# Kernel optimization log

Hardware: AMD Instinct MI355X
Metric: run time of the kernel (lower is better)

The kernel has to match this reference:

```python
import jax, jax.numpy as jnp
import numpy as np

D = 1024
H = 16
HD = D // H
FF = 4 * D
EPS = 1e-6


def layernorm(x, g, b):
    mu = jnp.mean(x, axis=-1, keepdims=True)
    var = jnp.mean((x - mu) ** 2, axis=-1, keepdims=True)
    return (x - mu) * jax.lax.rsqrt(var + EPS) * g + b


def setup_inputs() -> dict:
    key = jax.random.key(0)
    ks = jax.random.split(key, 12)
    s = 0.02
    return {
        "x": jax.random.normal(ks[0], (8, 1024, D), dtype=jnp.float32),
        "qkv_w": jax.random.normal(ks[1], (3 * D, D), dtype=jnp.float32) * s,
        "qkv_b": jnp.zeros((3 * D,), dtype=jnp.float32),
        "proj_w": jax.random.normal(ks[2], (D, D), dtype=jnp.float32) * s,
        "proj_b": jnp.zeros((D,), dtype=jnp.float32),
        "fc1_w": jax.random.normal(ks[3], (FF, D), dtype=jnp.float32) * s,
        "fc1_b": jnp.zeros((FF,), dtype=jnp.float32),
        "fc2_w": jax.random.normal(ks[4], (D, FF), dtype=jnp.float32) * s,
        "fc2_b": jnp.zeros((D,), dtype=jnp.float32),
        "ln1_g": jnp.ones((D,), dtype=jnp.float32),
        "ln1_b": jnp.zeros((D,), dtype=jnp.float32),
        "ln2_g": jnp.ones((D,), dtype=jnp.float32),
        "ln2_b": jnp.zeros((D,), dtype=jnp.float32),
    }


def reference(x, qkv_w, qkv_b, proj_w, proj_b, fc1_w, fc1_b, fc2_w, fc2_b,
              ln1_g, ln1_b, ln2_g, ln2_b):
    B, S, _ = x.shape
    # attention branch
    h = layernorm(x, ln1_g, ln1_b)
    qkv = h @ qkv_w.T + qkv_b                      # [B,S,3D]
    qkv = qkv.reshape(B, S, 3, H, HD)
    q, k, v = qkv[:, :, 0], qkv[:, :, 1], qkv[:, :, 2]  # [B,S,H,HD]
    scores = jnp.einsum('bshd,bthd->bhst', q, k) * (HD ** -0.5)
    attn = jax.nn.softmax(scores, axis=-1)
    ctx = jnp.einsum('bhst,bthd->bshd', attn, v).reshape(B, S, D)
    x = x + ctx @ proj_w.T + proj_b
    # mlp branch
    h = layernorm(x, ln2_g, ln2_b)
    h = jax.nn.gelu(h @ fc1_w.T + fc1_b, approximate=False)
    x = x + h @ fc2_w.T + fc2_b
    return x
```

## Files before the change

kernel.cpp:

```cpp
#include <hip/hip_runtime.h>
#include <stdint.h>

typedef unsigned short u16;
typedef __attribute__((ext_vector_type(8))) short bf16x8;
typedef __attribute__((ext_vector_type(4))) float f32x4;

__device__ __forceinline__ u16 f2bf(float f) {
    union { float f; uint32_t u; } v; v.f = f;
    uint32_t r = (v.u + 0x7FFFu + ((v.u >> 16) & 1u)) >> 16;
    return (u16)r;
}

__global__ __launch_bounds__(256) void cvt_kernel(const float* __restrict__ in,
                                                  u16* __restrict__ out, int n4) {
    int i = blockIdx.x * 256 + threadIdx.x;
    if (i < n4) {
        float4 v = ((const float4*)in)[i];
        uint2 o;
        o.x = (uint32_t)f2bf(v.x) | ((uint32_t)f2bf(v.y) << 16);
        o.y = (uint32_t)f2bf(v.z) | ((uint32_t)f2bf(v.w) << 16);
        ((uint2*)out)[i] = o;
    }
}

__global__ __launch_bounds__(256) void ln_kernel(const float* __restrict__ x,
                                                 const float* __restrict__ g,
                                                 const float* __restrict__ beta,
                                                 u16* __restrict__ out) {
    int row = blockIdx.x;
    int tid = threadIdx.x;
    const float4 v = ((const float4*)(x + (size_t)row * 1024))[tid];
    float s  = v.x + v.y + v.z + v.w;
    float sq = v.x*v.x + v.y*v.y + v.z*v.z + v.w*v.w;
    #pragma unroll
    for (int off = 32; off; off >>= 1) {
        s  += __shfl_xor(s,  off, 64);
        sq += __shfl_xor(sq, off, 64);
    }
    __shared__ float rs[4], rq[4];
    int w = tid >> 6;
    if ((tid & 63) == 0) { rs[w] = s; rq[w] = sq; }
    __syncthreads();
    s  = rs[0] + rs[1] + rs[2] + rs[3];
    sq = rq[0] + rq[1] + rq[2] + rq[3];
    float mu   = s * (1.0f / 1024.0f);
    float var  = sq * (1.0f / 1024.0f) - mu * mu;
    float rstd = rsqrtf(var + 1e-6f);
    float4 gv = ((const float4*)g)[tid];
    float4 bv = ((const float4*)beta)[tid];
    uint2 o;
    o.x = (uint32_t)f2bf((v.x - mu) * rstd * gv.x + bv.x) |
          ((uint32_t)f2bf((v.y - mu) * rstd * gv.y + bv.y) << 16);
    o.y = (uint32_t)f2bf((v.z - mu) * rstd * gv.z + bv.z) |
          ((uint32_t)f2bf((v.w - mu) * rstd * gv.w + bv.w) << 16);
    ((uint2*)(out + (size_t)row * 1024))[tid] = o;
}

template<int ACT, int RES, int OUTBF>
__global__ __launch_bounds__(256) void gemm_kernel(
    const u16* __restrict__ A, const u16* __restrict__ W,
    const float* __restrict__ bias, const float* __restrict__ res,
    void* __restrict__ Cout, int M, int N, int K)
{
    const int LDT = 72;
    __shared__ u16 sA[128 * LDT];
    __shared__ u16 sB[128 * LDT];
    int tid = threadIdx.x;
    int lane = tid & 63, wid = tid >> 6;
    int wm = wid >> 1, wn = wid & 1;
    int ntiles = N >> 7;
    int m0 = (blockIdx.x / ntiles) << 7;
    int n0 = (blockIdx.x % ntiles) << 7;
    int q = lane & 15, g = lane >> 4;

    f32x4 acc[4][4];
    #pragma unroll
    for (int i = 0; i < 4; i++)
        #pragma unroll
        for (int j = 0; j < 4; j++)
            acc[i][j] = (f32x4){0.f, 0.f, 0.f, 0.f};

    for (int k0 = 0; k0 < K; k0 += 64) {
        __syncthreads();
        #pragma unroll
        for (int p = 0; p < 4; p++) {
            int flat = (p * 256 + tid) * 8;
            int r = flat >> 6, c = flat & 63;
            uint4 av = *(const uint4*)(A + (size_t)(m0 + r) * K + k0 + c);
            *(uint4*)(sA + r * LDT + c) = av;
            uint4 bv = *(const uint4*)(W + (size_t)(n0 + r) * K + k0 + c);
            *(uint4*)(sB + r * LDT + c) = bv;
        }
        __syncthreads();
        #pragma unroll
        for (int ks = 0; ks < 2; ks++) {
            bf16x8 af[4], bf[4];
            #pragma unroll
            for (int i = 0; i < 4; i++) {
                af[i] = *(const bf16x8*)(sA + (wm * 64 + i * 16 + q) * LDT + ks * 32 + g * 8);
                bf[i] = *(const bf16x8*)(sB + (wn * 64 + i * 16 + q) * LDT + ks * 32 + g * 8);
            }
            #pragma unroll
            for (int i = 0; i < 4; i++)
                #pragma unroll
                for (int j = 0; j < 4; j++)
                    acc[i][j] = __builtin_amdgcn_mfma_f32_16x16x32_bf16(af[i], bf[j], acc[i][j], 0, 0, 0);
        }
    }

    #pragma unroll
    for (int i = 0; i < 4; i++) {
        #pragma unroll
        for (int j = 0; j < 4; j++) {
            int col = n0 + wn * 64 + j * 16 + q;
            float bz = bias[col];
            #pragma unroll
            for (int r = 0; r < 4; r++) {
                int row = m0 + wm * 64 + i * 16 + g * 4 + r;
                float v = acc[i][j][r] + bz;
                if (ACT == 1) v = 0.5f * v * (1.0f + erff(v * 0.70710678118654752f));
                if (RES) v += res[(size_t)row * N + col];
                if (OUTBF) ((u16*)Cout)[(size_t)row * N + col] = f2bf(v);
                else       ((float*)Cout)[(size_t)row * N + col] = v;
            }
        }
    }
}

__global__ __launch_bounds__(256) void attn_kernel(const u16* __restrict__ qkv,
                                                   u16* __restrict__ ctx) {
    int bid = blockIdx.x;
    int qt = bid & 15;
    int h  = (bid >> 4) & 15;
    int b  = bid >> 8;
    int tid = threadIdx.x, lane = tid & 63, w = tid >> 6;
    int q = lane & 15, g = lane >> 4;

    __shared__ u16 sQ[64 * 72];
    __shared__ u16 sK[32 * 72];
    __shared__ u16 sVT[64 * 40];

    const size_t tokBase = ((size_t)b * 1024) * 3072 + (size_t)h * 64;

    #pragma unroll
    for (int p = 0; p < 2; p++) {
        int flat = (p * 256 + tid) * 8;
        int r = flat >> 6, c = flat & 63;
        uint4 v = *(const uint4*)(qkv + tokBase + (size_t)(qt * 64 + r) * 3072 + c);
        *(uint4*)(sQ + r * 72 + c) = v;
    }
    __syncthreads();
    bf16x8 qf0 = *(const bf16x8*)(sQ + (w * 16 + q) * 72 + g * 8);
    bf16x8 qf1 = *(const bf16x8*)(sQ + (w * 16 + q) * 72 + 32 + g * 8);

    float m_run = -1e30f, l_run = 0.0f;
    f32x4 o[4];
    #pragma unroll
    for (int n = 0; n < 4; n++) o[n] = (f32x4){0.f, 0.f, 0.f, 0.f};

    for (int kt = 0; kt < 32; kt++) {
        __syncthreads();
        {
            int r = tid >> 3, c = (tid & 7) * 8;
            uint4 v = *(const uint4*)(qkv + tokBase + (size_t)(kt * 32 + r) * 3072 + 1024 + c);
            *(uint4*)(sK + r * 72 + c) = v;
        }
        #pragma unroll
        for (int p = 0; p < 2; p++) {
            int flat = (p * 256 + tid) * 4;
            int key = flat >> 6, c = flat & 63;
            const u16* src = qkv + tokBase + (size_t)(kt * 32 + key) * 3072 + 2048 + c;
            #pragma unroll
            for (int j = 0; j < 4; j++) sVT[(c + j) * 40 + key] = src[j];
        }
        __syncthreads();

        f32x4 s0 = (f32x4){0.f, 0.f, 0.f, 0.f}, s1 = s0;
        {
            bf16x8 k00 = *(const bf16x8*)(sK + (q) * 72 + g * 8);
            bf16x8 k01 = *(const bf16x8*)(sK + (q) * 72 + 32 + g * 8);
            s0 = __builtin_amdgcn_mfma_f32_16x16x32_bf16(k00, qf0, s0, 0, 0, 0);
            s0 = __builtin_amdgcn_mfma_f32_16x16x32_bf16(k01, qf1, s0, 0, 0, 0);
            bf16x8 k10 = *(const bf16x8*)(sK + (16 + q) * 72 + g * 8);
            bf16x8 k11 = *(const bf16x8*)(sK + (16 + q) * 72 + 32 + g * 8);
            s1 = __builtin_amdgcn_mfma_f32_16x16x32_bf16(k10, qf0, s1, 0, 0, 0);
            s1 = __builtin_amdgcn_mfma_f32_16x16x32_bf16(k11, qf1, s1, 0, 0, 0);
        }
        float ps[8];
        #pragma unroll
        for (int r = 0; r < 4; r++) { ps[r] = s0[r] * 0.125f; ps[4 + r] = s1[r] * 0.125f; }
        float tm = ps[0];
        #pragma unroll
        for (int i = 1; i < 8; i++) tm = fmaxf(tm, ps[i]);
        tm = fmaxf(tm, __shfl_xor(tm, 16, 64));
        tm = fmaxf(tm, __shfl_xor(tm, 32, 64));
        float nm = fmaxf(m_run, tm);
        float f = __expf(m_run - nm);
        float ts = 0.0f;
        #pragma unroll
        for (int i = 0; i < 8; i++) { ps[i] = __expf(ps[i] - nm); ts += ps[i]; }
        ts += __shfl_xor(ts, 16, 64);
        ts += __shfl_xor(ts, 32, 64);
        l_run = l_run * f + ts;
        m_run = nm;

        bf16x8 pf;
        #pragma unroll
        for (int j = 0; j < 8; j++) {
            int src = q + 16 * (2 * (g & 1) + (j >> 2));
            float a  = __shfl(ps[j & 3], src, 64);
            float bb = __shfl(ps[4 + (j & 3)], src, 64);
            float pv = (g >> 1) ? bb : a;
            pf[j] = (short)f2bf(pv);
        }
        float fr[4];
        #pragma unroll
        for (int r = 0; r < 4; r++) fr[r] = __shfl(f, g * 4 + r, 64);
        #pragma unroll
        for (int n = 0; n < 4; n++)
            #pragma unroll
            for (int r = 0; r < 4; r++) o[n][r] *= fr[r];
        #pragma unroll
        for (int n = 0; n < 4; n++) {
            bf16x8 vf = *(const bf16x8*)(sVT + (n * 16 + q) * 40 + g * 8);
            o[n] = __builtin_amdgcn_mfma_f32_16x16x32_bf16(pf, vf, o[n], 0, 0, 0);
        }
    }

    float inv = 1.0f / l_run;
    float ir[4];
    #pragma unroll
    for (int r = 0; r < 4; r++) ir[r] = __shfl(inv, g * 4 + r, 64);
    size_t outBase = ((size_t)b * 1024 + qt * 64 + w * 16) * 1024 + (size_t)h * 64;
    #pragma unroll
    for (int n = 0; n < 4; n++)
        #pragma unroll
        for (int r = 0; r < 4; r++)
            ctx[outBase + (size_t)(g * 4 + r) * 1024 + n * 16 + q] = f2bf(o[n][r] * ir[r]);
}

extern "C" void kernel_launch(void* const* d_in, const int* in_sizes, int n_in,
                              void* d_out, int out_size, void* d_ws, size_t ws_size,
                              hipStream_t stream) {
    const float* x      = (const float*)d_in[0];
    const float* qkv_w  = (const float*)d_in[1];
    const float* qkv_b  = (const float*)d_in[2];
    const float* proj_w = (const float*)d_in[3];
    const float* proj_b = (const float*)d_in[4];
    const float* fc1_w  = (const float*)d_in[5];
    const float* fc1_b  = (const float*)d_in[6];
    const float* fc2_w  = (const float*)d_in[7];
    const float* fc2_b  = (const float*)d_in[8];
    const float* ln1_g  = (const float*)d_in[9];
    const float* ln1_b  = (const float*)d_in[10];
    const float* ln2_g  = (const float*)d_in[11];
    const float* ln2_b  = (const float*)d_in[12];
    float* out = (float*)d_out;

    char* ws = (char*)d_ws;
    u16* wq = (u16*)(ws);
    u16* wp = (u16*)(ws + 6291456);
    u16* w1 = (u16*)(ws + 8388608);
    u16* w2 = (u16*)(ws + 16777216);
    char* pool = ws + 25165824;
    u16* hbuf = (u16*)(pool);
    u16* qkvb = (u16*)(pool + 16777216);
    u16* ctxb = (u16*)(pool);
    u16* h2b  = (u16*)(pool + 16777216);
    u16* a1b  = (u16*)(pool + 33554432);

    cvt_kernel<<<3072, 256, 0, stream>>>(qkv_w, wq, 786432);
    cvt_kernel<<<1024, 256, 0, stream>>>(proj_w, wp, 262144);
    cvt_kernel<<<4096, 256, 0, stream>>>(fc1_w, w1, 1048576);
    cvt_kernel<<<4096, 256, 0, stream>>>(fc2_w, w2, 1048576);

    ln_kernel<<<8192, 256, 0, stream>>>(x, ln1_g, ln1_b, hbuf);
    gemm_kernel<0,0,1><<<64 * 24, 256, 0, stream>>>(hbuf, wq, qkv_b, nullptr, qkvb, 8192, 3072, 1024);
    attn_kernel<<<2048, 256, 0, stream>>>(qkvb, ctxb);
    gemm_kernel<0,1,0><<<64 * 8, 256, 0, stream>>>(ctxb, wp, proj_b, x, out, 8192, 1024, 1024);
    ln_kernel<<<8192, 256, 0, stream>>>(out, ln2_g, ln2_b, h2b);
    gemm_kernel<1,0,1><<<64 * 32, 256, 0, stream>>>(h2b, w1, fc1_b, nullptr, a1b, 8192, 4096, 1024);
    gemm_kernel<0,1,0><<<64 * 8, 256, 0, stream>>>(a1b, w2, fc2_b, out, out, 8192, 1024, 4096);
}
```

Measured before the change: 646.5 us.

## Use direct global-to-LDS loads in GEMM and streamline attention softmax

```diff
diff --git a/kernel.cpp b/kernel.cpp
--- a/kernel.cpp
+++ b/kernel.cpp
@@ -3,12 +3,19 @@
 
 typedef unsigned short u16;
 typedef __attribute__((ext_vector_type(8))) short bf16x8;
+typedef __attribute__((ext_vector_type(4))) short bf16x4;
 typedef __attribute__((ext_vector_type(4))) float f32x4;
 
 __device__ __forceinline__ u16 f2bf(float f) {
     union { float f; uint32_t u; } v; v.f = f;
     uint32_t r = (v.u + 0x7FFFu + ((v.u >> 16) & 1u)) >> 16;
     return (u16)r;
+}
+
+__device__ __forceinline__ void g2l16(const u16* g, u16* l) {
+    __builtin_amdgcn_global_load_lds(
+        (const __attribute__((address_space(1))) uint32_t*)g,
+        (__attribute__((address_space(3))) uint32_t*)l, 16, 0, 0);
 }
 
 __global__ __launch_bounds__(256) void cvt_kernel(const float* __restrict__ in,
@@ -62,9 +69,8 @@
     const float* __restrict__ bias, const float* __restrict__ res,
     void* __restrict__ Cout, int M, int N, int K)
 {
-    const int LDT = 72;
-    __shared__ u16 sA[128 * LDT];
-    __shared__ u16 sB[128 * LDT];
+    __shared__ u16 sA[128 * 64];
+    __shared__ u16 sB[128 * 64];
     int tid = threadIdx.x;
     int lane = tid & 63, wid = tid >> 6;
     int wm = wid >> 1, wn = wid & 1;
@@ -83,28 +89,26 @@
     for (int k0 = 0; k0 < K; k0 += 64) {
         __syncthreads();
         #pragma unroll
-        for (int p = 0; p < 4; p++) {
-            int flat = (p * 256 + tid) * 8;
-            int r = flat >> 6, c = flat & 63;
-            uint4 av = *(const uint4*)(A + (size_t)(m0 + r) * K + k0 + c);
-            *(uint4*)(sA + r * LDT + c) = av;
-            uint4 bv = *(const uint4*)(W + (size_t)(n0 + r) * K + k0 + c);
-            *(uint4*)(sB + r * LDT + c) = bv;
+        for (int c = 0; c < 4; c++) {
+            int flat = ((c * 4 + wid) * 64 + lane) * 8;
+            int r = flat >> 6, cc = flat & 63;
+            g2l16(A + (size_t)(m0 + r) * K + k0 + cc, sA + (c * 4 + wid) * 512);
+            g2l16(W + (size_t)(n0 + r) * K + k0 + cc, sB + (c * 4 + wid) * 512);
         }
         __syncthreads();
         #pragma unroll
         for (int ks = 0; ks < 2; ks++) {
-            bf16x8 af[4], bf[4];
+            bf16x8 af[4], bfr[4];
             #pragma unroll
             for (int i = 0; i < 4; i++) {
-                af[i] = *(const bf16x8*)(sA + (wm * 64 + i * 16 + q) * LDT + ks * 32 + g * 8);
-                bf[i] = *(const bf16x8*)(sB + (wn * 64 + i * 16 + q) * LDT + ks * 32 + g * 8);
+                af[i]  = *(const bf16x8*)(sA + (wm * 64 + i * 16 + q) * 64 + ks * 32 + g * 8);
+                bfr[i] = *(const bf16x8*)(sB + (wn * 64 + i * 16 + q) * 64 + ks * 32 + g * 8);
             }
             #pragma unroll
             for (int i = 0; i < 4; i++)
                 #pragma unroll
                 for (int j = 0; j < 4; j++)
-                    acc[i][j] = __builtin_amdgcn_mfma_f32_16x16x32_bf16(af[i], bf[j], acc[i][j], 0, 0, 0);
+                    acc[i][j] = __builtin_amdgcn_mfma_f32_16x16x32_bf16(af[i], bfr[j], acc[i][j], 0, 0, 0);
         }
     }
 
@@ -138,9 +142,10 @@
 
     __shared__ u16 sQ[64 * 72];
     __shared__ u16 sK[32 * 72];
-    __shared__ u16 sVT[64 * 40];
+    __shared__ u16 sVT[64 * 36];
 
     const size_t tokBase = ((size_t)b * 1024) * 3072 + (size_t)h * 64;
+    const float SC = 0.125f * 1.44269504088896f;
 
     #pragma unroll
     for (int p = 0; p < 2; p++) {
@@ -158,20 +163,24 @@
     #pragma unroll
     for (int n = 0; n < 4; n++) o[n] = (f32x4){0.f, 0.f, 0.f, 0.f};
 
+    int kr = tid >> 3, kc = (tid & 7) * 8;
+    int kperm = ((kr >> 2) & 3) * 8 + (kr >> 4) * 4 + (kr & 3);
+
     for (int kt = 0; kt < 32; kt++) {
         __syncthreads();
         {
-            int r = tid >> 3, c = (tid & 7) * 8;
-            uint4 v = *(const uint4*)(qkv + tokBase + (size_t)(kt * 32 + r) * 3072 + 1024 + c);
-            *(uint4*)(sK + r * 72 + c) = v;
+            uint4 v = *(const uint4*)(qkv + tokBase + (size_t)(kt * 32 + kperm) * 3072 + 1024 + kc);
+            *(uint4*)(sK + kr * 72 + kc) = v;
         }
         #pragma unroll
         for (int p = 0; p < 2; p++) {
             int flat = (p * 256 + tid) * 4;
-            int key = flat >> 6, c = flat & 63;
-            const u16* src = qkv + tokBase + (size_t)(kt * 32 + key) * 3072 + 2048 + c;
-            #pragma unroll
-            for (int j = 0; j < 4; j++) sVT[(c + j) * 40 + key] = src[j];
+            int key = flat >> 6, cc = flat & 63;
+            ushort4 vv = *(const ushort4*)(qkv + tokBase + (size_t)(kt * 32 + key) * 3072 + 2048 + cc);
+            sVT[(cc + 0) * 36 + key] = vv.x;
+            sVT[(cc + 1) * 36 + key] = vv.y;
+            sVT[(cc + 2) * 36 + key] = vv.z;
+            sVT[(cc + 3) * 36 + key] = vv.w;
         }
         __syncthreads();
 
@@ -188,41 +197,45 @@
         }
         float ps[8];
         #pragma unroll
-        for (int r = 0; r < 4; r++) { ps[r] = s0[r] * 0.125f; ps[4 + r] = s1[r] * 0.125f; }
+        for (int r = 0; r < 4; r++) { ps[r] = s0[r] * SC; ps[4 + r] = s1[r] * SC; }
         float tm = ps[0];
         #pragma unroll
         for (int i = 1; i < 8; i++) tm = fmaxf(tm, ps[i]);
         tm = fmaxf(tm, __shfl_xor(tm, 16, 64));
         tm = fmaxf(tm, __shfl_xor(tm, 32, 64));
-        float nm = fmaxf(m_run, tm);
-        float f = __expf(m_run - nm);
+
+        if (!__all(tm - m_run <= 8.0f)) {
+            float nm = fmaxf(m_run, tm);
+            float f = exp2f(m_run - nm);
+            float fr[4];
+            #pragma unroll
+            for (int r = 0; r < 4; r++) fr[r] = __shfl(f, g * 4 + r, 64);
+            #pragma unroll
+            for (int n = 0; n < 4; n++)
+                #pragma unroll
+                for (int r = 0; r < 4; r++) o[n][r] *= fr[r];
+            l_run *= f;
+            m_run = nm;
+        }
+
         float ts = 0.0f;
         #pragma unroll
-        for (int i = 0; i < 8; i++) { ps[i] = __expf(ps[i] - nm); ts += ps[i]; }
+        for (int i = 0; i < 8; i++) { ps[i] = exp2f(ps[i] - m_run); ts += ps[i]; }
         ts += __shfl_xor(ts, 16, 64);
         ts += __shfl_xor(ts, 32, 64);
-        l_run = l_run * f + ts;
-        m_run = nm;
+        l_run += ts;
 
         bf16x8 pf;
         #pragma unroll
-        for (int j = 0; j < 8; j++) {
-            int src = q + 16 * (2 * (g & 1) + (j >> 2));
-            float a  = __shfl(ps[j & 3], src, 64);
-            float bb = __shfl(ps[4 + (j & 3)], src, 64);
-            float pv = (g >> 1) ? bb : a;
-            pf[j] = (short)f2bf(pv);
-        }
-        float fr[4];
-        #pragma unroll
-        for (int r = 0; r < 4; r++) fr[r] = __shfl(f, g * 4 + r, 64);
-        #pragma unroll
-        for (int n = 0; n < 4; n++)
-            #pragma unroll
-            for (int r = 0; r < 4; r++) o[n][r] *= fr[r];
+        for (int j = 0; j < 8; j++) pf[j] = (short)f2bf(ps[j]);
+
         #pragma unroll
         for (int n = 0; n < 4; n++) {
-            bf16x8 vf = *(const bf16x8*)(sVT + (n * 16 + q) * 40 + g * 8);
+            bf16x4 vlo = *(const bf16x4*)(sVT + (n * 16 + q) * 36 + g * 8);
+            bf16x4 vhi = *(const bf16x4*)(sVT + (n * 16 + q) * 36 + g * 8 + 4);
+            bf16x8 vf;
+            #pragma unroll
+            for (int j = 0; j < 4; j++) { vf[j] = vlo[j]; vf[4 + j] = vhi[j]; }
             o[n] = __builtin_amdgcn_mfma_f32_16x16x32_bf16(pf, vf, o[n], 0, 0, 0);
         }
     }
```

After: 591.1 us. -8.6%, faster.
